# Performance work log

Hardware: AMD Instinct MI355X
Metric: run time of the kernel (lower is better)

The kernel has to match this reference:

```python
import jax, jax.numpy as jnp
import numpy as np

H = 256   # hidden size
U = 10    # attention units


def _lstm_cell(xt, h, c, Wih, Whh, bih, bhh):
    # PyTorch gate order: i, f, g, o
    gates = xt @ Wih.T + h @ Whh.T + bih + bhh          # [B, 4H]
    i, f, g, o = jnp.split(gates, 4, axis=-1)
    i = jax.nn.sigmoid(i); f = jax.nn.sigmoid(f)
    g = jnp.tanh(g);       o = jax.nn.sigmoid(o)
    c = f * c + i * g
    h = o * jnp.tanh(c)
    return h, c


def setup_inputs() -> dict:
    key = jax.random.key(0)
    ks = jax.random.split(key, 12)
    B, S = 512, 256
    s = 1.0 / np.sqrt(H)
    x = jax.random.normal(ks[0], (B, S), dtype=jnp.float32)
    y = jax.random.randint(ks[1], (B, S), 0, S, dtype=jnp.int64)
    return {
        "x": x,
        "y": y,
        "enc_Wih": jax.random.uniform(ks[2], (4 * H, 1), jnp.float32, -s, s),
        "enc_Whh": jax.random.uniform(ks[3], (4 * H, H), jnp.float32, -s, s),
        "enc_bih": jax.random.uniform(ks[4], (4 * H,), jnp.float32, -s, s),
        "enc_bhh": jax.random.uniform(ks[5], (4 * H,), jnp.float32, -s, s),
        "dec_Wih": jax.random.uniform(ks[6], (4 * H, H + 1), jnp.float32, -s, s),
        "dec_Whh": jax.random.uniform(ks[7], (4 * H, H), jnp.float32, -s, s),
        "dec_bih": jax.random.uniform(ks[8], (4 * H,), jnp.float32, -s, s),
        "dec_bhh": jax.random.uniform(ks[9], (4 * H,), jnp.float32, -s, s),
        "att_W1": jax.random.uniform(ks[10], (U, H), jnp.float32, -s, s),
        "att_W2": jax.random.uniform(ks[11], (U, H), jnp.float32, -s, s),
        "att_V": jax.random.uniform(jax.random.fold_in(key, 99), (1, U), jnp.float32, -s, s),
    }


def reference(x, y, enc_Wih, enc_Whh, enc_bih, enc_bhh,
              dec_Wih, dec_Whh, dec_bih, dec_bhh,
              att_W1, att_W2, att_V):
    B, S = x.shape

    # ---- Encoder: LSTM over sequence of scalar inputs ----
    def enc_step(carry, xt):  # xt: [B, 1]
        h, c = carry
        h, c = _lstm_cell(xt, h, c, enc_Wih, enc_Whh, enc_bih, enc_bhh)
        return (h, c), h

    h0 = jnp.zeros((B, H), x.dtype)
    (hN, cN), enc_out_t = jax.lax.scan(enc_step, (h0, h0), x.T[:, :, None])
    enc_out = jnp.transpose(enc_out_t, (1, 0, 2))            # [B, S, H]

    # precompute W1 @ encoder_hidden (same math, hoisted out of loop)
    encW1 = jnp.einsum('bsh,uh->bsu', enc_out, att_W1)       # [B, S, U]

    # ---- Decoder loop (teacher forcing with ratio 1.0) ----
    def dec_step(carry, y_t):
        h, c, dec_in = carry                                  # dec_in: [B, 1]
        u = jnp.tanh(encW1 + (h @ att_W2.T)[:, None, :])      # [B, S, U]
        logits = jnp.einsum('bsu,ou->bso', u, att_V)[..., 0]  # [B, S]
        aj = jax.nn.softmax(logits, axis=1)
        di = jnp.einsum('bs,bsh->bh', aj, enc_out)            # [B, H]
        lstm_in = jnp.concatenate([di, dec_in], axis=1)       # [B, H+1]
        h, c = _lstm_cell(lstm_in, h, c, dec_Wih, dec_Whh, dec_bih, dec_bhh)
        pred = jnp.argmax(logits, axis=1)                     # [B]
        logp = jax.nn.log_softmax(logits, axis=1)
        loss_t = -jnp.mean(jnp.take_along_axis(logp, y_t[:, None], axis=1))
        dec_in_next = jnp.take_along_axis(x, y_t[:, None], axis=1)  # teacher force
        return (h, c, dec_in_next), (pred, loss_t)

    dec_in0 = jnp.zeros((B, 1), x.dtype)
    _, (preds, losses) = jax.lax.scan(dec_step, (hN, cN, dec_in0), y.T)
    outputs = preds[:, :, None].astype(jnp.int64)             # [S, B, 1]
    batch_loss = jnp.sum(losses) / B
    return outputs, batch_loss
```

## Files before the change

kernel.cpp:

```cpp
#include <hip/hip_runtime.h>
#include <cmath>

__device__ __forceinline__ double dexp_(double x) {
    x = fmin(fmax(x, -64.0), 64.0);
    double w = x * 1.4426950408889634;
    double n = rint(w);
    double u = (w - n) * 0.6931471805599453;
    double p = 1.0 + u * (1.0 + u * (0.5 + u * (1.6666666666666666e-01 +
               u * (4.1666666666666664e-02 + u * (8.3333333333333332e-03 +
               u * (1.3888888888888889e-03 + u * (1.9841269841269841e-04 +
               u * (2.4801587301587302e-05 + u * (2.7557319223985893e-06 +
               u * (2.7557319223985888e-07 + u * 2.5052108385441720e-08))))))))));
    return ldexp(p, (int)n);
}
__device__ __forceinline__ double dtanh_(double x) {
    double ax = fabs(x);
    double e = dexp_(2.0 * ax);
    double t = 1.0 - 2.0 / (e + 1.0);
    return copysign(t, x);
}
__device__ __forceinline__ double dsig_(double x) {
    return 1.0 / (1.0 + dexp_(-x));
}

__device__ __forceinline__ void fma_range(
    const float* __restrict__ wcol, int row0, const float* __restrict__ xsrc,
    int k_beg, int k_end, double& A0, double& A1, double& A2, double& A3)
{
    for (int k0 = k_beg; k0 < k_end; k0 += 8) {
        float4 w[8];
        #pragma unroll
        for (int i = 0; i < 8; ++i)
            w[i] = *(const float4*)&wcol[(row0 + k0 + i) * 1024];
        float4 xa = *(const float4*)&xsrc[k0];
        float4 xb = *(const float4*)&xsrc[k0 + 4];
        float xv[8] = {xa.x, xa.y, xa.z, xa.w, xb.x, xb.y, xb.z, xb.w};
        float s0 = 0.f, s1 = 0.f, s2 = 0.f, s3 = 0.f;
        #pragma unroll
        for (int i = 0; i < 8; ++i) {
            s0 = fmaf(w[i].x, xv[i], s0);
            s1 = fmaf(w[i].y, xv[i], s1);
            s2 = fmaf(w[i].z, xv[i], s2);
            s3 = fmaf(w[i].w, xv[i], s3);
        }
        A0 += (double)s0; A1 += (double)s1;
        A2 += (double)s2; A3 += (double)s3;
    }
}

__global__ __launch_bounds__(256) void prep_kernel(
    const float* __restrict__ eWih, const float* __restrict__ eWhh,
    const float* __restrict__ ebih, const float* __restrict__ ebhh,
    const float* __restrict__ dWih, const float* __restrict__ dWhh,
    const float* __restrict__ dbih, const float* __restrict__ dbhh,
    float* __restrict__ WencR, double* __restrict__ bencR,
    float* __restrict__ WdecR, double* __restrict__ bdecR)
{
    const int n_enc = 257 * 1024;
    const int n_dec = 513 * 1024;
    const int total = n_enc + n_dec + 2048;
    for (int idx = blockIdx.x * blockDim.x + threadIdx.x; idx < total;
         idx += gridDim.x * blockDim.x) {
        if (idx < n_enc) {
            int k = idx >> 10, c = idx & 1023;
            int j = c >> 2, g = c & 3, r = g * 256 + j;
            WencR[idx] = (k == 0) ? eWih[r] : eWhh[r * 256 + (k - 1)];
        } else if (idx < n_enc + n_dec) {
            int i2 = idx - n_enc;
            int k = i2 >> 10, c = i2 & 1023;
            int j = c >> 2, g = c & 3, r = g * 256 + j;
            WdecR[i2] = (k < 257) ? dWih[r * 257 + k] : dWhh[r * 256 + (k - 257)];
        } else {
            int c = idx - n_enc - n_dec;
            if (c < 1024) {
                int r = (c & 3) * 256 + (c >> 2);
                bencR[c] = (double)ebih[r] + (double)ebhh[r];
            } else {
                int c2 = c - 1024;
                int r = (c2 & 3) * 256 + (c2 >> 2);
                bdecR[c2] = (double)dbih[r] + (double)dbhh[r];
            }
        }
    }
}

__global__ __launch_bounds__(512) void enc_fused_kernel(
    const float* __restrict__ x, const float* __restrict__ W,
    const double* __restrict__ bR, float* __restrict__ enc_out,
    float* __restrict__ c_st)
{
    __shared__ float h_lds[2][2][256];
    __shared__ float xs[2][2];
    const int tid = threadIdx.x;
    const int bb  = tid >> 8;
    const int j   = tid & 255;
    const int b0g = blockIdx.x * 2;
    const int b   = b0g + bb;

    h_lds[0][bb][j] = 0.0f;
    float c_f = 0.f;
    const double bi = bR[j * 4 + 0], bf = bR[j * 4 + 1];
    const double bg = bR[j * 4 + 2], bo = bR[j * 4 + 3];
    const float* wcol = W + j * 4;

    for (int t = 0; t < 256; ++t) {
        const int cur = t & 1, nxt = cur ^ 1;
        if (tid < 2) xs[cur][tid] = x[(b0g + tid) * 256 + t];
        __syncthreads();

        double A0 = 0, A1 = 0, A2 = 0, A3 = 0;
        const float* hh = h_lds[cur][bb];
        fma_range(wcol, 1, hh, 0, 256, A0, A1, A2, A3);
        {
            float4 w = *(const float4*)&wcol[0];
            float xv = xs[cur][bb];
            A0 += (double)(w.x * xv); A1 += (double)(w.y * xv);
            A2 += (double)(w.z * xv); A3 += (double)(w.w * xv);
        }

        double iv = dsig_(A0 + bi);
        double fv = dsig_(A1 + bf);
        double gv = dtanh_(A2 + bg);
        double ov = dsig_(A3 + bo);
        double c = fv * (double)c_f + iv * gv;
        c_f = (float)c;
        float hv = (float)(ov * dtanh_(c));
        enc_out[(long)b * 65536 + t * 256 + j] = hv;
        h_lds[nxt][bb][j] = hv;
        __syncthreads();
    }

    c_st[(long)b * 256 + j] = c_f;
}

__global__ __launch_bounds__(256) void encW1_kernel(
    const float* __restrict__ enc_out, const float* __restrict__ W1,
    double* __restrict__ encW1d)
{
    __shared__ float sa[64][260];
    __shared__ float sw[10][257];
    const int tid = threadIdx.x;
    const int m0 = blockIdx.x * 64;
    #pragma unroll
    for (int i = 0; i < 16; ++i) {
        int idx = tid + i * 256;
        int row = idx >> 6;
        int c4 = (idx & 63) * 4;
        const float4 v = *(const float4*)&enc_out[(long)(m0 + row) * 256 + c4];
        *(float4*)&sa[row][c4] = v;
    }
    for (int i = tid; i < 2560; i += 256) sw[i >> 8][i & 255] = W1[i];
    __syncthreads();
    for (int o = tid; o < 640; o += 256) {
        int r = o / 10;
        int u = o - r * 10;
        double acc = 0.0;
        #pragma unroll 4
        for (int k = 0; k < 256; ++k)
            acc += (double)sa[r][k] * (double)sw[u][k];
        encW1d[(long)(m0 + r) * 10 + u] = acc;
    }
}

__global__ __launch_bounds__(256) void transpose_kernel(float* __restrict__ eo)
{
    __shared__ float ta[32][33], tb[32][33];
    const int tid = threadIdx.x;
    const int r   = tid >> 3;
    const int c4  = (tid & 7) * 4;
    float* base = eo + (long)blockIdx.x * 65536;

    for (int ti = 0; ti < 8; ++ti) {
        for (int tj = ti; tj < 8; ++tj) {
            float4 va = *(const float4*)&base[(ti * 32 + r) * 256 + tj * 32 + c4];
            ta[r][c4 + 0] = va.x; ta[r][c4 + 1] = va.y;
            ta[r][c4 + 2] = va.z; ta[r][c4 + 3] = va.w;
            if (tj > ti) {
                float4 vb = *(const float4*)&base[(tj * 32 + r) * 256 + ti * 32 + c4];
                tb[r][c4 + 0] = vb.x; tb[r][c4 + 1] = vb.y;
                tb[r][c4 + 2] = vb.z; tb[r][c4 + 3] = vb.w;
            }
            __syncthreads();
            {
                float4 w;
                w.x = ta[c4 + 0][r]; w.y = ta[c4 + 1][r];
                w.z = ta[c4 + 2][r]; w.w = ta[c4 + 3][r];
                *(float4*)&base[(tj * 32 + r) * 256 + ti * 32 + c4] = w;
            }
            if (tj > ti) {
                float4 w;
                w.x = tb[c4 + 0][r]; w.y = tb[c4 + 1][r];
                w.z = tb[c4 + 2][r]; w.w = tb[c4 + 3][r];
                *(float4*)&base[(ti * 32 + r) * 256 + tj * 32 + c4] = w;
            }
            __syncthreads();
        }
    }
}

__global__ __launch_bounds__(256, 2) void dec_fused_kernel(
    const double* __restrict__ encW1d, const float* __restrict__ enc_out,
    const float* __restrict__ W2, const float* __restrict__ V,
    const float* __restrict__ x, const int* __restrict__ y,
    const float* __restrict__ W, const double* __restrict__ bR,
    const float* __restrict__ c_init, float* __restrict__ logp_buf,
    float* __restrict__ out_pred)
{
    __shared__ float h_lds[2][256];
    __shared__ float di_lds[256];
    __shared__ float e_lds[256];
    __shared__ float rcpZ_s;
    __shared__ float din_s;
    __shared__ double s_V[12];
    __shared__ double s_W2h[12];
    __shared__ double s_ld[256];
    __shared__ double s_red[4];
    __shared__ int s_redi[4];
    __shared__ double s_maxd;
    __shared__ int s_am;

    const int tid  = threadIdx.x;
    const int j    = tid;
    const int wid  = tid >> 6;
    const int lane = tid & 63;
    const int b    = blockIdx.x;

    if (tid < 10) s_V[tid] = (double)V[tid];
    h_lds[0][j] = enc_out[(long)b * 65536 + j * 256 + 255];
    float c_f = c_init[(long)b * 256 + j];
    const double bi = bR[j * 4 + 0], bf = bR[j * 4 + 1];
    const double bg = bR[j * 4 + 2], bo = bR[j * 4 + 3];
    const float* wcol = W + j * 4;
    __syncthreads();

    for (int t = 0; t < 256; ++t) {
        const int cur = t & 1, nxt = cur ^ 1;
        const float* hh = h_lds[cur];

        for (int u = wid; u < 10; u += 4) {
            double p = 0.0;
            #pragma unroll
            for (int i = 0; i < 4; ++i) {
                int k = lane + i * 64;
                p += (double)W2[u * 256 + k] * (double)hh[k];
            }
            #pragma unroll
            for (int off = 32; off >= 1; off >>= 1) p += __shfl_down(p, off, 64);
            if (lane == 0) s_W2h[u] = p;
        }
        __syncthreads();

        const double* eW = encW1d + ((long)b * 256 + j) * 10;
        double l = 0.0;
        #pragma unroll
        for (int u = 0; u < 10; ++u) l += s_V[u] * dtanh_(eW[u] + s_W2h[u]);
        s_ld[j] = l;

        {
            double v = l; int idx = j;
            #pragma unroll
            for (int off = 32; off >= 1; off >>= 1) {
                double v2 = __shfl_down(v, off, 64);
                int i2 = __shfl_down(idx, off, 64);
                if (v2 > v || (v2 == v && i2 < idx)) { v = v2; idx = i2; }
            }
            if (lane == 0) { s_red[wid] = v; s_redi[wid] = idx; }
        }
        __syncthreads();
        if (tid == 0) {
            double v = s_red[0]; int idx = s_redi[0];
            #pragma unroll
            for (int w2 = 1; w2 < 4; ++w2) {
                if (s_red[w2] > v || (s_red[w2] == v && s_redi[w2] < idx)) {
                    v = s_red[w2]; idx = s_redi[w2];
                }
            }
            s_maxd = v; s_am = idx;
        }
        __syncthreads();

        double e = dexp_(l - s_maxd);
        e_lds[j] = (float)e;
        {
            double v = e;
            #pragma unroll
            for (int off = 32; off >= 1; off >>= 1) v += __shfl_down(v, off, 64);
            if (lane == 0) s_red[wid] = v;
        }
        __syncthreads();
        if (tid == 0) {
            double Z = s_red[0] + s_red[1] + s_red[2] + s_red[3];
            rcpZ_s = (float)(1.0 / Z);
            out_pred[t * 512 + b] = (float)s_am;
            int yv = y[b * 256 + t];
            logp_buf[t * 512 + b] = (float)(s_ld[yv] - s_maxd - log(Z));
        } else if (tid == 1) {
            float dv = 0.0f;
            if (t > 0) { int yi = y[b * 256 + (t - 1)]; dv = x[b * 256 + yi]; }
            din_s = dv;
        }
        __syncthreads();

        {
            const float* ep = enc_out + (long)b * 65536 + j * 256;
            float acc0 = 0.f, acc1 = 0.f, acc2 = 0.f, acc3 = 0.f;
            for (int s2 = 0; s2 < 256; s2 += 4) {
                float4 v = *(const float4*)&ep[s2];
                acc0 += e_lds[s2 + 0] * v.x;
                acc1 += e_lds[s2 + 1] * v.y;
                acc2 += e_lds[s2 + 2] * v.z;
                acc3 += e_lds[s2 + 3] * v.w;
            }
            di_lds[j] = ((acc0 + acc1) + (acc2 + acc3)) * rcpZ_s;
        }
        __syncthreads();

        double A0 = 0, A1 = 0, A2 = 0, A3 = 0;

        fma_range(wcol, 0, di_lds, 0, 256, A0, A1, A2, A3);
        {
            float4 w = *(const float4*)&wcol[256 * 1024];
            float xv = din_s;
            A0 += (double)(w.x * xv); A1 += (double)(w.y * xv);
            A2 += (double)(w.z * xv); A3 += (double)(w.w * xv);
        }
        fma_range(wcol, 257, hh, 0, 256, A0, A1, A2, A3);

        double iv = dsig_(A0 + bi);
        double fv = dsig_(A1 + bf);
        double gv = dtanh_(A2 + bg);
        double ov = dsig_(A3 + bo);
        double c = fv * (double)c_f + iv * gv;
        c_f = (float)c;
        h_lds[nxt][j] = (float)(ov * dtanh_(c));
        __syncthreads();
    }
}

__global__ __launch_bounds__(256) void loss_kernel(
    const float* __restrict__ logp_buf, float* __restrict__ out)
{
    const int tid = threadIdx.x;
    double acc = 0.0;
    for (int i = tid; i < 131072; i += 256) acc += (double)logp_buf[i];
    __shared__ double s_red[4];
    const int wid = tid >> 6, lane = tid & 63;
    #pragma unroll
    for (int off = 32; off >= 1; off >>= 1) acc += __shfl_down(acc, off, 64);
    if (lane == 0) s_red[wid] = acc;
    __syncthreads();
    if (tid == 0) {
        out[131072] = (float)(-(s_red[0] + s_red[1] + s_red[2] + s_red[3])
                              / (512.0 * 512.0));
    }
}

extern "C" void kernel_launch(void* const* d_in, const int* in_sizes, int n_in,
                              void* d_out, int out_size, void* d_ws, size_t ws_size,
                              hipStream_t stream)
{
    const float* x    = (const float*)d_in[0];
    const int*   y    = (const int*)  d_in[1];
    const float* eWih = (const float*)d_in[2];
    const float* eWhh = (const float*)d_in[3];
    const float* ebih = (const float*)d_in[4];
    const float* ebhh = (const float*)d_in[5];
    const float* dWih = (const float*)d_in[6];
    const float* dWhh = (const float*)d_in[7];
    const float* dbih = (const float*)d_in[8];
    const float* dbhh = (const float*)d_in[9];
    const float* W1   = (const float*)d_in[10];
    const float* W2   = (const float*)d_in[11];
    const float* V    = (const float*)d_in[12];

    double* encW1d = (double*)d_ws;
    double* bencR  = encW1d + 1310720;
    double* bdecR  = bencR + 1024;
    float* enc_out = (float*)(bdecR + 1024);
    float* c_st    = enc_out + 33554432;
    float* hzero   = c_st + 131072;
    float* hd      = hzero + 131072;
    float* dibuf   = hd + 262144;
    float* logp    = dibuf + 131072;
    float* WencR   = logp + 131072;
    float* WdecR   = WencR + 263168;

    float* out = (float*)d_out;

    prep_kernel<<<512, 256, 0, stream>>>(eWih, eWhh, ebih, ebhh,
                                         dWih, dWhh, dbih, dbhh,
                                         WencR, bencR, WdecR, bdecR);

    enc_fused_kernel<<<256, 512, 0, stream>>>(x, WencR, bencR, enc_out, c_st);

    encW1_kernel<<<2048, 256, 0, stream>>>(enc_out, W1, encW1d);

    transpose_kernel<<<512, 256, 0, stream>>>(enc_out);

    dec_fused_kernel<<<512, 256, 0, stream>>>(encW1d, enc_out, W2, V, x, y,
                                              WdecR, bdecR, c_st, logp, out);

    loss_kernel<<<1, 256, 0, stream>>>(logp, out);
}
```

Measured before the change: 17.64 ms.

## Give each encoder block one batch row and cache decoder attention operands in LDS

The encoder now runs one batch row per 256-thread block instead of two rows per 512-thread block. It reads x straight from global memory and drops the trailing barrier, relying on the double-buffered hidden state to stay safe. The decoder preloads its per-batch encW1 slice (transposed) and the W2 matrix into shared memory once. This removes repeated global loads on every step of the time loop. The cost is more LDS per decoder block, which may lower occupancy, and twice as many encoder blocks.

```diff
diff --git a/kernel.cpp b/kernel.cpp
--- a/kernel.cpp
+++ b/kernel.cpp
@@ -84,20 +84,17 @@
     }
 }
 
-__global__ __launch_bounds__(512) void enc_fused_kernel(
+__global__ __launch_bounds__(256, 2) void enc_fused_kernel(
     const float* __restrict__ x, const float* __restrict__ W,
     const double* __restrict__ bR, float* __restrict__ enc_out,
     float* __restrict__ c_st)
 {
-    __shared__ float h_lds[2][2][256];
-    __shared__ float xs[2][2];
+    __shared__ float h_lds[2][256];
     const int tid = threadIdx.x;
-    const int bb  = tid >> 8;
-    const int j   = tid & 255;
-    const int b0g = blockIdx.x * 2;
-    const int b   = b0g + bb;
-
-    h_lds[0][bb][j] = 0.0f;
+    const int j   = tid;
+    const int b   = blockIdx.x;
+
+    h_lds[0][j] = 0.0f;
     float c_f = 0.f;
     const double bi = bR[j * 4 + 0], bf = bR[j * 4 + 1];
     const double bg = bR[j * 4 + 2], bo = bR[j * 4 + 3];
@@ -105,15 +102,14 @@
 
     for (int t = 0; t < 256; ++t) {
         const int cur = t & 1, nxt = cur ^ 1;
-        if (tid < 2) xs[cur][tid] = x[(b0g + tid) * 256 + t];
         __syncthreads();
 
         double A0 = 0, A1 = 0, A2 = 0, A3 = 0;
-        const float* hh = h_lds[cur][bb];
+        const float* hh = h_lds[cur];
         fma_range(wcol, 1, hh, 0, 256, A0, A1, A2, A3);
         {
             float4 w = *(const float4*)&wcol[0];
-            float xv = xs[cur][bb];
+            float xv = x[b * 256 + t];
             A0 += (double)(w.x * xv); A1 += (double)(w.y * xv);
             A2 += (double)(w.z * xv); A3 += (double)(w.w * xv);
         }
@@ -126,8 +122,7 @@
         c_f = (float)c;
         float hv = (float)(ov * dtanh_(c));
         enc_out[(long)b * 65536 + t * 256 + j] = hv;
-        h_lds[nxt][bb][j] = hv;
-        __syncthreads();
+        h_lds[nxt][j] = hv;
     }
 
     c_st[(long)b * 256 + j] = c_f;
@@ -206,6 +201,8 @@
     const float* __restrict__ c_init, float* __restrict__ logp_buf,
     float* __restrict__ out_pred)
 {
+    __shared__ double eW_lds[10][260];
+    __shared__ float  W2_lds[10][256];
     __shared__ float h_lds[2][256];
     __shared__ float di_lds[256];
     __shared__ float e_lds[256];
@@ -226,6 +223,11 @@
     const int b    = blockIdx.x;
 
     if (tid < 10) s_V[tid] = (double)V[tid];
+    for (int i = tid; i < 2560; i += 256) {
+        int s = i / 10, u = i - s * 10;
+        eW_lds[u][s] = encW1d[(long)b * 2560 + i];
+        W2_lds[i >> 8][i & 255] = W2[i];
+    }
     h_lds[0][j] = enc_out[(long)b * 65536 + j * 256 + 255];
     float c_f = c_init[(long)b * 256 + j];
     const double bi = bR[j * 4 + 0], bf = bR[j * 4 + 1];
@@ -242,7 +244,7 @@
             #pragma unroll
             for (int i = 0; i < 4; ++i) {
                 int k = lane + i * 64;
-                p += (double)W2[u * 256 + k] * (double)hh[k];
+                p += (double)W2_lds[u][k] * (double)hh[k];
             }
             #pragma unroll
             for (int off = 32; off >= 1; off >>= 1) p += __shfl_down(p, off, 64);
@@ -250,10 +252,9 @@
         }
         __syncthreads();
 
-        const double* eW = encW1d + ((long)b * 256 + j) * 10;
         double l = 0.0;
         #pragma unroll
-        for (int u = 0; u < 10; ++u) l += s_V[u] * dtanh_(eW[u] + s_W2h[u]);
+        for (int u = 0; u < 10; ++u) l += s_V[u] * dtanh_(eW_lds[u][j] + s_W2h[u]);
         s_ld[j] = l;
 
         {
@@ -391,7 +392,7 @@
                                          dWih, dWhh, dbih, dbhh,
                                          WencR, bencR, WdecR, bdecR);
 
-    enc_fused_kernel<<<256, 512, 0, stream>>>(x, WencR, bencR, enc_out, c_st);
+    enc_fused_kernel<<<512, 256, 0, stream>>>(x, WencR, bencR, enc_out, c_st);
 
     encW1_kernel<<<2048, 256, 0, stream>>>(enc_out, W1, encW1d);
 
```

After: 17.37 ms, median of 2. About the same (-1.5%).
